# Optimization experiments

Measured on AMD Instinct MI355X. Metric: run time of the kernel, lower is better.

The kernel has to match this reference:

```python
import jax, jax.numpy as jnp
import numpy as np

N, K, D = 100000, 16, 128

def setup_inputs() -> dict:
    key = jax.random.key(0)
    k1, k2, k3, k4, k5 = jax.random.split(key, 5)
    s = 1.0 / np.sqrt(D)  # nn.Linear default init scale
    return {
        "h": jax.random.normal(k1, (N, D), dtype=jnp.float32),
        "nbr_idx": jax.random.randint(k2, (N, K), 0, N, dtype=jnp.int64),
        "nbr_w": jax.random.uniform(k3, (N, K), dtype=jnp.float32),
        "w_self": jax.random.uniform(k4, (D, D), minval=-s, maxval=s, dtype=jnp.float32),
        "w_nei": jax.random.uniform(k5, (D, D), minval=-s, maxval=s, dtype=jnp.float32),
        "ln_gamma": jnp.ones((D,), dtype=jnp.float32),
        "ln_beta": jnp.zeros((D,), dtype=jnp.float32),
    }

def layer_norm(x, gamma, beta, eps=1e-5):
    mu = jnp.mean(x, axis=-1, keepdims=True)
    var = jnp.mean(jnp.square(x - mu), axis=-1, keepdims=True)
    return (x - mu) * jax.lax.rsqrt(var + eps) * gamma + beta

def reference(h, nbr_idx, nbr_w, w_self, w_nei, ln_gamma, ln_beta):
    # gather neighbor features: [N, K, D]
    nei = h[nbr_idx]
    # weighted sum over neighbors -> [N, D]
    agg = jnp.einsum('nk,nkd->nd', nbr_w, nei)
    # dual linear (nn.Linear applies x @ W.T) + exact (erf) GELU
    out = jax.nn.gelu(h @ w_self.T + agg @ w_nei.T, approximate=False)
    # dropout is identity at inference; then LayerNorm
    return layer_norm(out, ln_gamma, ln_beta)
```

## Files before the change

kernel.cpp:

```cpp
#include <hip/hip_runtime.h>
#include <hip/hip_bf16.h>
#include <math.h>

#define DFEAT 128
#define KNBR  16
#define NPB   64

typedef __attribute__((ext_vector_type(8))) short short8;
typedef __attribute__((ext_vector_type(4))) float f32x4;

__device__ __forceinline__ unsigned short f2bf(float x) {
    union { float f; unsigned u; } v; v.f = x;
    unsigned r = v.u + 0x7FFFu + ((v.u >> 16) & 1u);
    return (unsigned short)(r >> 16);
}
__device__ __forceinline__ float bf2f(unsigned short u) {
    union { unsigned u; float f; } v; v.u = ((unsigned)u) << 16; return v.f;
}

__global__ __launch_bounds__(256)
void prep_kernel(const float* __restrict__ h,
                 const float* __restrict__ wself,
                 const float* __restrict__ wnei,
                 unsigned short* __restrict__ h16,
                 unsigned short* __restrict__ wcat,
                 int ntot8) {
    const int t = blockIdx.x * 256 + threadIdx.x;
    if (t < 4096) {
        const int base = t * 8;
        const int j = base >> 8;
        const int d0 = base & 255;
        const float* src = (d0 < DFEAT) ? (wself + j * DFEAT + d0)
                                        : (wnei  + j * DFEAT + (d0 - DFEAT));
        float4 a = ((const float4*)src)[0], b = ((const float4*)src)[1];
        short8 o;
        o[0] = f2bf(a.x); o[1] = f2bf(a.y); o[2] = f2bf(a.z); o[3] = f2bf(a.w);
        o[4] = f2bf(b.x); o[5] = f2bf(b.y); o[6] = f2bf(b.z); o[7] = f2bf(b.w);
        *(short8*)(wcat + base) = o;
        return;
    }
    const long u = (long)t - 4096;
    if (u >= ntot8) return;
    const float4* src = (const float4*)(h + u * 8);
    float4 a = src[0], b = src[1];
    short8 o;
    o[0] = f2bf(a.x); o[1] = f2bf(a.y); o[2] = f2bf(a.z); o[3] = f2bf(a.w);
    o[4] = f2bf(b.x); o[5] = f2bf(b.y); o[6] = f2bf(b.z); o[7] = f2bf(b.w);
    *(short8*)(h16 + u * 8) = o;
}

template<int H16>
__global__ __launch_bounds__(256, 4)
void sage_fused_kernel(const float* __restrict__ h,
                       const unsigned short* __restrict__ h16,
                       const int* __restrict__ nbr32,
                       const float* __restrict__ nbrw,
                       const unsigned short* __restrict__ wcat,
                       const float* __restrict__ gamma,
                       const float* __restrict__ beta,
                       float* __restrict__ out,
                       int N) {
    __shared__ __align__(16) unsigned short xlds[NPB][256];

    const int tid = threadIdx.x;
    const int nb  = blockIdx.x * NPB;

    const bool idx64 = ((nbr32[1] | nbr32[3] | nbr32[5] | nbr32[7] |
                         nbr32[9] | nbr32[11] | nbr32[13] | nbr32[15]) == 0);

    const int l   = tid & 63;
    const int wvi = tid >> 6;
    const int q   = l & 15;
    const int gb  = l & 48;

    #pragma unroll 1
    for (int r = 0; r < 4; ++r) {
        const int i = wvi * 16 + (l >> 4) * 4 + r;
        int n = nb + i; if (n >= N) n = N - 1;

        short8 hv;
        float acc[8] = {0.f,0.f,0.f,0.f,0.f,0.f,0.f,0.f};

        if constexpr (H16) {
            const int e = n * KNBR + q;
            const int   myidx = __builtin_nontemporal_load(&nbr32[idx64 ? 2 * e : e]);
            const float myw   = __builtin_nontemporal_load(&nbrw[e]);

            hv = *(const short8*)(h16 + (long)n * DFEAT + q * 8);

            short8 nv[16];
            #pragma unroll
            for (int k = 0; k < 16; ++k) {
                int ik = __shfl(myidx, gb + k, 64);
                nv[k] = *(const short8*)(h16 + (long)ik * DFEAT + q * 8);
            }
            #pragma unroll
            for (int k = 0; k < 16; ++k) {
                float wk = __shfl(myw, gb + k, 64);
                #pragma unroll
                for (int d = 0; d < 8; ++d)
                    acc[d] += wk * bf2f((unsigned short)nv[k][d]);
            }
        } else {
            const float4* hrow = (const float4*)(h + (long)n * DFEAT + q * 8);
            float4 h0 = hrow[0], h1 = hrow[1];
            hv[0] = f2bf(h0.x); hv[1] = f2bf(h0.y); hv[2] = f2bf(h0.z); hv[3] = f2bf(h0.w);
            hv[4] = f2bf(h1.x); hv[5] = f2bf(h1.y); hv[6] = f2bf(h1.z); hv[7] = f2bf(h1.w);
            const int e0 = n * KNBR;
            #pragma unroll 4
            for (int k = 0; k < KNBR; ++k) {
                float w = nbrw[e0 + k];
                int idx = nbr32[idx64 ? 2 * (e0 + k) : (e0 + k)];
                const float4* nrow = (const float4*)(h + (long)idx * DFEAT + q * 8);
                float4 n0 = nrow[0], n1 = nrow[1];
                acc[0] += w * n0.x; acc[1] += w * n0.y;
                acc[2] += w * n0.z; acc[3] += w * n0.w;
                acc[4] += w * n1.x; acc[5] += w * n1.y;
                acc[6] += w * n1.z; acc[7] += w * n1.w;
            }
        }

        *(short8*)&xlds[i][(q ^ (i & 7)) * 8] = hv;
        short8 ab;
        #pragma unroll
        for (int d = 0; d < 8; ++d) ab[d] = f2bf(acc[d]);
        *(short8*)&xlds[i][((16 + q) ^ (i & 7)) * 8] = ab;
    }
    __syncthreads();

    const int wv  = wvi;
    const int col = l & 15;
    const int kg  = l >> 4;

    f32x4 acc2[4][2];
    #pragma unroll
    for (int s = 0; s < 4; ++s)
        #pragma unroll
        for (int t = 0; t < 2; ++t)
            acc2[s][t] = (f32x4){0.f, 0.f, 0.f, 0.f};

    const unsigned short* wbase0 = wcat + (wv * 32 + col) * 256 + kg * 8;
    const unsigned short* wbase1 = wbase0 + 16 * 256;

    #pragma unroll
    for (int kk = 0; kk < 8; ++kk) {
        short8 b0 = *(const short8*)(wbase0 + kk * 32);
        short8 b1 = *(const short8*)(wbase1 + kk * 32);
        #pragma unroll
        for (int s = 0; s < 4; ++s) {
            const int row = s * 16 + col;
            const int c = (kk * 4 + kg) ^ (row & 7);
            short8 a = *(const short8*)&xlds[row][c * 8];
            acc2[s][0] = __builtin_amdgcn_mfma_f32_16x16x32_bf16(a, b0, acc2[s][0], 0, 0, 0);
            acc2[s][1] = __builtin_amdgcn_mfma_f32_16x16x32_bf16(a, b1, acc2[s][1], 0, 0, 0);
        }
    }

    float y[4][2][4];
    #pragma unroll
    for (int s = 0; s < 4; ++s)
        #pragma unroll
        for (int t = 0; t < 2; ++t)
            #pragma unroll
            for (int r = 0; r < 4; ++r) {
                float x = acc2[s][t][r];
                y[s][t][r] = 0.5f * x * (1.0f + erff(x * 0.70710678118654752f));
            }

    __syncthreads();

    float* lsum = (float*)&xlds[0][0];
    float* lsq  = lsum + 4 * NPB;

    #pragma unroll
    for (int s = 0; s < 4; ++s) {
        f32x4 sm, sq;
        #pragma unroll
        for (int r = 0; r < 4; ++r) {
            float a0 = y[s][0][r], a1 = y[s][1][r];
            sm[r] = a0 + a1;
            sq[r] = a0 * a0 + a1 * a1;
        }
        #pragma unroll
        for (int m = 1; m < 16; m <<= 1) {
            #pragma unroll
            for (int r = 0; r < 4; ++r) {
                sm[r] += __shfl_xor(sm[r], m, 64);
                sq[r] += __shfl_xor(sq[r], m, 64);
            }
        }
        if (col == 0) {
            *(f32x4*)&lsum[wv * NPB + s * 16 + kg * 4] = sm;
            *(f32x4*)&lsq [wv * NPB + s * 16 + kg * 4] = sq;
        }
    }
    __syncthreads();

    const float g0  = gamma[wv * 32 + col];
    const float g1  = gamma[wv * 32 + 16 + col];
    const float be0 = beta [wv * 32 + col];
    const float be1 = beta [wv * 32 + 16 + col];

    #pragma unroll
    for (int s = 0; s < 4; ++s) {
        f32x4 sm = {0.f,0.f,0.f,0.f}, sq = {0.f,0.f,0.f,0.f};
        #pragma unroll
        for (int u = 0; u < 4; ++u) {
            f32x4 a = *(const f32x4*)&lsum[u * NPB + s * 16 + kg * 4];
            f32x4 b = *(const f32x4*)&lsq [u * NPB + s * 16 + kg * 4];
            sm += a; sq += b;
        }
        #pragma unroll
        for (int r = 0; r < 4; ++r) {
            const int i = s * 16 + kg * 4 + r;
            const int n = nb + i;
            if (n < N) {
                float mean = sm[r] * (1.0f / 128.0f);
                float var  = sq[r] * (1.0f / 128.0f) - mean * mean;
                float rstd = rsqrtf(var + 1e-5f);
                long o = (long)n * DFEAT + wv * 32 + col;
                __builtin_nontemporal_store((y[s][0][r] - mean) * rstd * g0 + be0, &out[o]);
                __builtin_nontemporal_store((y[s][1][r] - mean) * rstd * g1 + be1, &out[o + 16]);
            }
        }
    }
}

extern "C" void kernel_launch(void* const* d_in, const int* in_sizes, int n_in,
                              void* d_out, int out_size, void* d_ws, size_t ws_size,
                              hipStream_t stream) {
    const float* h     = (const float*)d_in[0];
    const int*   nbr   = (const int*)  d_in[1];
    const float* nbrw  = (const float*)d_in[2];
    const float* wself = (const float*)d_in[3];
    const float* wnei  = (const float*)d_in[4];
    const float* gamma = (const float*)d_in[5];
    const float* beta  = (const float*)d_in[6];
    const int N = in_sizes[0] / DFEAT;

    unsigned short* wcat = (unsigned short*)d_ws;
    unsigned short* h16  = (unsigned short*)((char*)d_ws + 65536);
    const size_t need = 65536 + (size_t)N * DFEAT * sizeof(unsigned short);

    const int blocks = (N + NPB - 1) / NPB;
    if (ws_size >= need) {
        const int ntot8 = N * DFEAT / 8;
        const int pthreads = 4096 + ntot8;
        prep_kernel<<<(pthreads + 255) / 256, 256, 0, stream>>>(h, wself, wnei, h16, wcat, ntot8);
        sage_fused_kernel<1><<<blocks, 256, 0, stream>>>(h, h16, nbr, nbrw, wcat,
                                                         gamma, beta, (float*)d_out, N);
    } else {
        prep_kernel<<<(4096 + 255) / 256, 256, 0, stream>>>(h, wself, wnei, h16, wcat, 0);
        sage_fused_kernel<0><<<blocks, 256, 0, stream>>>(h, (const unsigned short*)nullptr,
                                                         nbr, nbrw, wcat,
                                                         gamma, beta, (float*)d_out, N);
    }
}
```

Before: 95.79 us.

## Software-pipeline neighbor gathers with double buffers across node rows

In the bf16 path, the gather loop over four nodes per lane group is restructured into a double-buffered pipeline. Half of a node's neighbor rows are fetched into one register buffer while the other buffer is reduced, and the next node's gathers are issued before the current node's accumulation finishes. Index, weight and self-row loads for all four nodes are hoisted up front. The prep kernel also switches to nontemporal loads and stores for the h-to-bf16 conversion. The aim is to hide gather latency, at the cost of more live registers, which may hurt occupancy under launch_bounds(256,4).

```diff
diff --git a/kernel.cpp b/kernel.cpp
--- a/kernel.cpp
+++ b/kernel.cpp
@@ -32,21 +32,21 @@
         const int d0 = base & 255;
         const float* src = (d0 < DFEAT) ? (wself + j * DFEAT + d0)
                                         : (wnei  + j * DFEAT + (d0 - DFEAT));
-        float4 a = ((const float4*)src)[0], b = ((const float4*)src)[1];
+        f32x4 a = ((const f32x4*)src)[0], b = ((const f32x4*)src)[1];
         short8 o;
-        o[0] = f2bf(a.x); o[1] = f2bf(a.y); o[2] = f2bf(a.z); o[3] = f2bf(a.w);
-        o[4] = f2bf(b.x); o[5] = f2bf(b.y); o[6] = f2bf(b.z); o[7] = f2bf(b.w);
+        o[0] = f2bf(a[0]); o[1] = f2bf(a[1]); o[2] = f2bf(a[2]); o[3] = f2bf(a[3]);
+        o[4] = f2bf(b[0]); o[5] = f2bf(b[1]); o[6] = f2bf(b[2]); o[7] = f2bf(b[3]);
         *(short8*)(wcat + base) = o;
         return;
     }
     const long u = (long)t - 4096;
     if (u >= ntot8) return;
-    const float4* src = (const float4*)(h + u * 8);
-    float4 a = src[0], b = src[1];
+    f32x4 a = __builtin_nontemporal_load((const f32x4*)(h + u * 8));
+    f32x4 b = __builtin_nontemporal_load((const f32x4*)(h + u * 8) + 1);
     short8 o;
-    o[0] = f2bf(a.x); o[1] = f2bf(a.y); o[2] = f2bf(a.z); o[3] = f2bf(a.w);
-    o[4] = f2bf(b.x); o[5] = f2bf(b.y); o[6] = f2bf(b.z); o[7] = f2bf(b.w);
-    *(short8*)(h16 + u * 8) = o;
+    o[0] = f2bf(a[0]); o[1] = f2bf(a[1]); o[2] = f2bf(a[2]); o[3] = f2bf(a[3]);
+    o[4] = f2bf(b[0]); o[5] = f2bf(b[1]); o[6] = f2bf(b[2]); o[7] = f2bf(b[3]);
+    __builtin_nontemporal_store(o, (short8*)(h16 + u * 8));
 }
 
 template<int H16>
@@ -72,59 +72,89 @@
     const int wvi = tid >> 6;
     const int q   = l & 15;
     const int gb  = l & 48;
-
-    #pragma unroll 1
-    for (int r = 0; r < 4; ++r) {
-        const int i = wvi * 16 + (l >> 4) * 4 + r;
-        int n = nb + i; if (n >= N) n = N - 1;
-
-        short8 hv;
-        float acc[8] = {0.f,0.f,0.f,0.f,0.f,0.f,0.f,0.f};
-
-        if constexpr (H16) {
+    const int i0  = wvi * 16 + (l >> 4) * 4;
+
+    if constexpr (H16) {
+        int   nn[4]; int myidx[4]; float myw[4]; short8 hv[4];
+        #pragma unroll
+        for (int r = 0; r < 4; ++r) {
+            int n = nb + i0 + r; if (n >= N) n = N - 1;
+            nn[r] = n;
             const int e = n * KNBR + q;
-            const int   myidx = __builtin_nontemporal_load(&nbr32[idx64 ? 2 * e : e]);
-            const float myw   = __builtin_nontemporal_load(&nbrw[e]);
-
-            hv = *(const short8*)(h16 + (long)n * DFEAT + q * 8);
-
-            short8 nv[16];
-            #pragma unroll
-            for (int k = 0; k < 16; ++k) {
-                int ik = __shfl(myidx, gb + k, 64);
-                nv[k] = *(const short8*)(h16 + (long)ik * DFEAT + q * 8);
-            }
-            #pragma unroll
-            for (int k = 0; k < 16; ++k) {
-                float wk = __shfl(myw, gb + k, 64);
-                #pragma unroll
-                for (int d = 0; d < 8; ++d)
-                    acc[d] += wk * bf2f((unsigned short)nv[k][d]);
-            }
-        } else {
-            const float4* hrow = (const float4*)(h + (long)n * DFEAT + q * 8);
-            float4 h0 = hrow[0], h1 = hrow[1];
-            hv[0] = f2bf(h0.x); hv[1] = f2bf(h0.y); hv[2] = f2bf(h0.z); hv[3] = f2bf(h0.w);
-            hv[4] = f2bf(h1.x); hv[5] = f2bf(h1.y); hv[6] = f2bf(h1.z); hv[7] = f2bf(h1.w);
+            myidx[r] = __builtin_nontemporal_load(&nbr32[idx64 ? 2 * e : e]);
+            myw[r]   = __builtin_nontemporal_load(&nbrw[e]);
+        }
+        #pragma unroll
+        for (int r = 0; r < 4; ++r)
+            hv[r] = *(const short8*)(h16 + (long)nn[r] * DFEAT + q * 8);
+
+        short8 bufA[8], bufB[8];
+        float  acc[8];
+
+        #define ISSUE(BUF, r, hh)                                             \
+            _Pragma("unroll")                                                 \
+            for (int k8 = 0; k8 < 8; ++k8) {                                  \
+                int ik = __shfl(myidx[r], gb + (hh) * 8 + k8, 64);            \
+                BUF[k8] = *(const short8*)(h16 + (long)ik * DFEAT + q * 8);   \
+            }
+        #define CONSUME(BUF, r, hh)                                           \
+            _Pragma("unroll")                                                 \
+            for (int k8 = 0; k8 < 8; ++k8) {                                  \
+                float wk = __shfl(myw[r], gb + (hh) * 8 + k8, 64);            \
+                _Pragma("unroll")                                             \
+                for (int d = 0; d < 8; ++d)                                   \
+                    acc[d] += wk * bf2f((unsigned short)BUF[k8][d]);          \
+            }
+        #define RESET() { _Pragma("unroll") for (int d = 0; d < 8; ++d) acc[d] = 0.f; }
+        #define STORE(r) {                                                    \
+            const int i = i0 + (r);                                           \
+            *(short8*)&xlds[i][(q ^ (i & 7)) * 8] = hv[r];                    \
+            short8 ab;                                                        \
+            _Pragma("unroll") for (int d = 0; d < 8; ++d) ab[d] = f2bf(acc[d]); \
+            *(short8*)&xlds[i][((16 + q) ^ (i & 7)) * 8] = ab; }
+
+        ISSUE(bufA, 0, 0); ISSUE(bufB, 0, 1);
+        RESET(); CONSUME(bufA, 0, 0); ISSUE(bufA, 1, 0);
+                 CONSUME(bufB, 0, 1); ISSUE(bufB, 1, 1); STORE(0);
+        RESET(); CONSUME(bufA, 1, 0); ISSUE(bufA, 2, 0);
+                 CONSUME(bufB, 1, 1); ISSUE(bufB, 2, 1); STORE(1);
+        RESET(); CONSUME(bufA, 2, 0); ISSUE(bufA, 3, 0);
+                 CONSUME(bufB, 2, 1); ISSUE(bufB, 3, 1); STORE(2);
+        RESET(); CONSUME(bufA, 3, 0);
+                 CONSUME(bufB, 3, 1); STORE(3);
+        #undef ISSUE
+        #undef CONSUME
+        #undef RESET
+        #undef STORE
+    } else {
+        #pragma unroll 1
+        for (int r = 0; r < 4; ++r) {
+            const int i = i0 + r;
+            int n = nb + i; if (n >= N) n = N - 1;
+            short8 hv;
+            float acc[8] = {0.f,0.f,0.f,0.f,0.f,0.f,0.f,0.f};
+            const f32x4* hrow = (const f32x4*)(h + (long)n * DFEAT + q * 8);
+            f32x4 h0 = hrow[0], h1 = hrow[1];
+            hv[0] = f2bf(h0[0]); hv[1] = f2bf(h0[1]); hv[2] = f2bf(h0[2]); hv[3] = f2bf(h0[3]);
+            hv[4] = f2bf(h1[0]); hv[5] = f2bf(h1[1]); hv[6] = f2bf(h1[2]); hv[7] = f2bf(h1[3]);
             const int e0 = n * KNBR;
             #pragma unroll 4
             for (int k = 0; k < KNBR; ++k) {
                 float w = nbrw[e0 + k];
                 int idx = nbr32[idx64 ? 2 * (e0 + k) : (e0 + k)];
-                const float4* nrow = (const float4*)(h + (long)idx * DFEAT + q * 8);
-                float4 n0 = nrow[0], n1 = nrow[1];
-                acc[0] += w * n0.x; acc[1] += w * n0.y;
-                acc[2] += w * n0.z; acc[3] += w * n0.w;
-                acc[4] += w * n1.x; acc[5] += w * n1.y;
-                acc[6] += w * n1.z; acc[7] += w * n1.w;
-            }
-        }
-
-        *(short8*)&xlds[i][(q ^ (i & 7)) * 8] = hv;
-        short8 ab;
-        #pragma unroll
-        for (int d = 0; d < 8; ++d) ab[d] = f2bf(acc[d]);
-        *(short8*)&xlds[i][((16 + q) ^ (i & 7)) * 8] = ab;
+                const f32x4* nrow = (const f32x4*)(h + (long)idx * DFEAT + q * 8);
+                f32x4 n0 = nrow[0], n1 = nrow[1];
+                acc[0] += w * n0[0]; acc[1] += w * n0[1];
+                acc[2] += w * n0[2]; acc[3] += w * n0[3];
+                acc[4] += w * n1[0]; acc[5] += w * n1[1];
+                acc[6] += w * n1[2]; acc[7] += w * n1[3];
+            }
+            *(short8*)&xlds[i][(q ^ (i & 7)) * 8] = hv;
+            short8 ab;
+            #pragma unroll
+            for (int d = 0; d < 8; ++d) ab[d] = f2bf(acc[d]);
+            *(short8*)&xlds[i][((16 + q) ^ (i & 7)) * 8] = ab;
+        }
     }
     __syncthreads();
 
```

Result: no change. 94.52 us (-1.3%).
